# Performance work log

Measured on AMD Instinct MI355X. Metric: run time of the kernel, lower is better.

## Reference

```python
import jax, jax.numpy as jnp
import numpy as np

B, T, E, A = 512, 64, 1536, 6
STOCH, DETER, HID = 32, 512, 512
MIN_STD = 0.1
EPS = 1e-3  # LayerNorm eps in the torch module


def _ln(x, g, b):
    m = jnp.mean(x, -1, keepdims=True)
    v = jnp.var(x, -1, keepdims=True)
    return (x - m) * jax.lax.rsqrt(v + EPS) * g + b


def setup_inputs() -> dict:
    key = jax.random.key(0)
    ks = jax.random.split(key, 20)
    s = 0.02
    f32 = jnp.float32
    return {
        "embed": jax.random.normal(ks[0], (B, T, E), f32),
        "action": jax.random.normal(ks[1], (B, T, A), f32),
        "reset": jnp.zeros((B, T, 1), f32),
        "noise_post": jax.random.normal(ks[2], (T, B, STOCH), f32),
        "noise_prior": jax.random.normal(ks[3], (T, B, STOCH), f32),
        # params
        "W_inp": jax.random.normal(ks[4], (STOCH + A, HID), f32) * s,
        "g_inp": jnp.ones((HID,), f32),
        "b_inp": jnp.zeros((HID,), f32),
        "W_gru": jax.random.normal(ks[5], (HID + DETER, 3 * DETER), f32) * s,
        "W_img": jax.random.normal(ks[6], (DETER, HID), f32) * s,
        "g_img": jnp.ones((HID,), f32),
        "b_img": jnp.zeros((HID,), f32),
        "W_obs": jax.random.normal(ks[7], (DETER + E, HID), f32) * s,
        "g_obs": jnp.ones((HID,), f32),
        "b_obs": jnp.zeros((HID,), f32),
        "W_ims": jax.random.normal(ks[8], (HID, 2 * STOCH), f32) * s,
        "b_ims": jnp.zeros((2 * STOCH,), f32),
        "W_ostat": jax.random.normal(ks[9], (HID, 2 * STOCH), f32) * s,
        "b_ostat": jnp.zeros((2 * STOCH,), f32),
        "W_init": jax.random.normal(ks[10], (1, DETER), f32) * s,
    }


def reference(embed, action, reset, noise_post, noise_prior,
              W_inp, g_inp, b_inp, W_gru, W_img, g_img, b_img,
              W_obs, g_obs, b_obs, W_ims, b_ims, W_ostat, b_ostat, W_init):
    silu = jax.nn.silu

    def img_out(d):
        return silu(_ln(d @ W_img, g_img, b_img))

    def ims_stats(h):
        st = h @ W_ims + b_ims
        mean, std = jnp.split(st, 2, -1)
        return mean, jax.nn.softplus(std) + MIN_STD

    # initial='learned': deter0 = tanh(W); stoch0 = mode of prior dist = mean
    deter0 = jnp.tanh(W_init) * jnp.ones((B, 1), embed.dtype)  # [B, DETER]
    stoch0, _ = ims_stats(img_out(deter0))                     # [B, STOCH]

    def step(carry, xs):
        stoch, deter = carry
        a, e, r, npost, nprior = xs
        # reset handling: blend prev state with initial state
        a = a * (1.0 - r)
        deter = deter * (1.0 - r) + deter0 * r
        stoch = stoch * (1.0 - r) + stoch0 * r
        # img_step: input MLP
        x = silu(_ln(jnp.concatenate([stoch, a], -1) @ W_inp, g_inp, b_inp))
        # GRUCell (update_bias=-1, tanh cand, no norm)
        parts = jnp.concatenate([x, deter], -1) @ W_gru
        rg, cand, up = jnp.split(parts, 3, -1)
        rg = jax.nn.sigmoid(rg)
        cand = jnp.tanh(rg * cand)
        up = jax.nn.sigmoid(up - 1.0)
        deter_n = up * cand + (1.0 - up) * deter
        # prior stats + reparam sample
        p_mean, p_std = ims_stats(img_out(deter_n))
        p_stoch = p_mean + p_std * nprior
        # posterior (temp_post=True: concat deter with embed)
        h = silu(_ln(jnp.concatenate([deter_n, e], -1) @ W_obs, g_obs, b_obs))
        st = h @ W_ostat + b_ostat
        q_mean, q_std = jnp.split(st, 2, -1)
        q_std = jax.nn.softplus(q_std) + MIN_STD
        q_stoch = q_mean + q_std * npost
        out = jnp.concatenate([q_mean, q_std, q_stoch, p_mean, p_std, p_stoch, deter_n], -1)
        return (q_stoch, deter_n), out

    xs = (jnp.swapaxes(action, 0, 1), jnp.swapaxes(embed, 0, 1),
          jnp.swapaxes(reset, 0, 1), noise_post, noise_prior)
    _, outs = jax.lax.scan(step, (stoch0, deter0), xs)
    # [B, T, 6*STOCH + DETER]
    return jnp.swapaxes(outs, 0, 1)
```

## Files before the change

kernel.cpp:

```cpp
#include <hip/hip_runtime.h>
#include <stdint.h>

typedef unsigned short u16;
typedef unsigned int u32;
typedef __attribute__((ext_vector_type(8))) short bf16x8;
typedef __attribute__((ext_vector_type(4))) float f32x4;

#define DEV __device__ __forceinline__

#define NB 512
#define NT 64
#define NE 1536
#define NH 512
#define NS 32

static constexpr size_t OFF_EOBS   = 0;
static constexpr size_t OFF_XX     = OFF_EOBS + (size_t)NT*NB*512*4;
static constexpr size_t OFF_XD     = OFF_XX + (size_t)512*512*2;
static constexpr size_t OFF_DF     = OFF_XD + (size_t)2*512*512*2;
static constexpr size_t OFF_D0     = OFF_DF + (size_t)512*512*4;
static constexpr size_t OFF_S0     = OFF_D0 + 512*4;
static constexpr size_t OFF_WINPT  = OFF_S0 + 256;
static constexpr size_t OFF_WGRUT  = OFF_WINPT + (size_t)512*64*2;
static constexpr size_t OFF_WIMGT  = OFF_WGRUT + (size_t)1536*1024*2;
static constexpr size_t OFF_WOBSDT = OFF_WIMGT + (size_t)512*512*2;
static constexpr size_t OFF_WOBSET = OFF_WOBSDT + (size_t)512*512*2;
static constexpr size_t OFF_WIMST  = OFF_WOBSET + (size_t)512*1536*2;
static constexpr size_t OFF_WOSTT  = OFF_WIMST + (size_t)64*512*2;
static constexpr size_t WS_NEED    = OFF_WOSTT + (size_t)64*512*2;

DEV u16 f2b(float f) {
  u32 u = __builtin_bit_cast(u32, f);
  u32 r = (u + 0x7FFFu + ((u >> 16) & 1u)) >> 16;
  return (u16)r;
}
DEV float b2f(u16 h) { u32 u = (u32)h << 16; return __builtin_bit_cast(float, u); }
DEV u32 pk2(float a, float b) { return (u32)f2b(a) | ((u32)f2b(b) << 16); }
DEV float sigf(float x) { return 1.f / (1.f + __expf(-x)); }
DEV float siluf(float x) { return x * sigf(x); }
DEV float softplusf(float x) { return (x > 20.f) ? x : log1pf(__expf(x)); }
DEV f32x4 mfma16(bf16x8 a, bf16x8 b, f32x4 c) {
  return __builtin_amdgcn_mfma_f32_16x16x32_bf16(a, b, c, 0, 0, 0);
}
DEV size_t bswz(int colgrp, int kkmax, int kk, int lane) {
  return (((size_t)colgrp * kkmax + kk) * 64 + lane) * 8;
}

__global__ __launch_bounds__(256) void k_convert(
    const float* __restrict__ W_inp, const float* __restrict__ W_gru,
    const float* __restrict__ W_img, const float* __restrict__ W_obs,
    const float* __restrict__ W_ims, const float* __restrict__ W_ostat,
    char* __restrict__ ws) {
  u16* winpT  = (u16*)(ws + OFF_WINPT);
  u16* wgruT  = (u16*)(ws + OFF_WGRUT);
  u16* wimgT  = (u16*)(ws + OFF_WIMGT);
  u16* wobsdT = (u16*)(ws + OFF_WOBSDT);
  u16* wobseT = (u16*)(ws + OFF_WOBSET);
  u16* wimsT  = (u16*)(ws + OFF_WIMST);
  u16* wostT  = (u16*)(ws + OFF_WOSTT);
  int o = blockIdx.x * 256 + threadIdx.x;
  if (o < 32768) {
    int i = o & 7, lane = (o >> 3) & 63, rem = o >> 9;
    int kk = rem & 1, cg = rem >> 1;
    int col = cg*16 + (lane & 15), k = kk*32 + (lane >> 4)*8 + i;
    winpT[o] = (k < 38) ? f2b(W_inp[k*512 + col]) : (u16)0;
    return;
  }
  o -= 32768;
  if (o < 1572864) {
    int i = o & 7, lane = (o >> 3) & 63, rem = o >> 9;
    int kk = rem & 31, cg = rem >> 5;
    int col = cg*16 + (lane & 15), k = kk*32 + (lane >> 4)*8 + i;
    wgruT[o] = f2b(W_gru[(size_t)k*1536 + col]);
    return;
  }
  o -= 1572864;
  if (o < 262144) {
    int i = o & 7, lane = (o >> 3) & 63, rem = o >> 9;
    int kk = rem & 15, cg = rem >> 4;
    int col = cg*16 + (lane & 15), k = kk*32 + (lane >> 4)*8 + i;
    wimgT[o] = f2b(W_img[k*512 + col]);
    return;
  }
  o -= 262144;
  if (o < 262144) {
    int i = o & 7, lane = (o >> 3) & 63, rem = o >> 9;
    int kk = rem & 15, cg = rem >> 4;
    int col = cg*16 + (lane & 15), k = kk*32 + (lane >> 4)*8 + i;
    wobsdT[o] = f2b(W_obs[k*512 + col]);
    return;
  }
  o -= 262144;
  if (o < 786432) {
    int i = o & 7, lane = (o >> 3) & 63, rem = o >> 9;
    int kk = rem % 48, cg = rem / 48;
    int col = cg*16 + (lane & 15), k = kk*32 + (lane >> 4)*8 + i;
    wobseT[o] = f2b(W_obs[(size_t)(512 + k)*512 + col]);
    return;
  }
  o -= 786432;
  if (o < 32768) {
    int i = o & 7, lane = (o >> 3) & 63, rem = o >> 9;
    int kk = rem & 15, cg = rem >> 4;
    int col = cg*16 + (lane & 15), k = kk*32 + (lane >> 4)*8 + i;
    wimsT[o] = f2b(W_ims[k*64 + col]);
    return;
  }
  o -= 32768;
  {
    int i = o & 7, lane = (o >> 3) & 63, rem = o >> 9;
    int kk = rem & 15, cg = rem >> 4;
    int col = cg*16 + (lane & 15), k = kk*32 + (lane >> 4)*8 + i;
    wostT[o] = f2b(W_ostat[k*64 + col]);
  }
}

__global__ __launch_bounds__(256) void k_init_a(
    const float* __restrict__ W_init, const float* __restrict__ W_img,
    const float* __restrict__ g_img, const float* __restrict__ b_img,
    const float* __restrict__ W_ims, const float* __restrict__ b_ims,
    char* __restrict__ ws) {
  __shared__ float DL[512];
  __shared__ float HL[512];
  __shared__ float RED[256];
  float* d0 = (float*)(ws + OFF_D0);
  float* s0 = (float*)(ws + OFF_S0);
  const int t = threadIdx.x;
  for (int j = t; j < 512; j += 256) { float v = tanhf(W_init[j]); DL[j] = v; d0[j] = v; }
  __syncthreads();
  float pre0 = 0.f, pre1 = 0.f;
  for (int k = 0; k < 512; ++k) {
    float dv = DL[k];
    pre0 += dv * W_img[k*512 + t];
    pre1 += dv * W_img[k*512 + t + 256];
  }
  RED[t] = pre0 + pre1;
  __syncthreads();
  for (int s = 128; s > 0; s >>= 1) { if (t < s) RED[t] += RED[t + s]; __syncthreads(); }
  float m = RED[0] * (1.f/512.f);
  __syncthreads();
  RED[t] = pre0*pre0 + pre1*pre1;
  __syncthreads();
  for (int s = 128; s > 0; s >>= 1) { if (t < s) RED[t] += RED[t + s]; __syncthreads(); }
  float var = RED[0] * (1.f/512.f) - m*m;
  float inv = rsqrtf(var + 1e-3f);
  HL[t]       = siluf((pre0 - m)*inv*g_img[t] + b_img[t]);
  HL[t + 256] = siluf((pre1 - m)*inv*g_img[t+256] + b_img[t+256]);
  __syncthreads();
  if (t < 32) {
    float s = 0.f;
    for (int k = 0; k < 512; ++k) s += HL[k] * W_ims[k*64 + t];
    s0[t] = s + b_ims[t];
  }
}

__global__ __launch_bounds__(256) void k_phase1(
    const float* __restrict__ embed, char* __restrict__ ws) {
  const u16* wobse = (const u16*)(ws + OFF_WOBSET);
  float* eobs = (float*)(ws + OFF_EOBS);
  __shared__ u16 AL[32 * 40];
  const int tid = threadIdx.x;
  const int mb = blockIdx.x;
  const int w = tid >> 6, l = tid & 63, l15 = l & 15, lk = l >> 4;
  const f32x4 fz = {0.f, 0.f, 0.f, 0.f};
  f32x4 acc[2][8];
  for (int a = 0; a < 2; ++a) for (int f = 0; f < 8; ++f) acc[a][f] = fz;
  const int srow = tid >> 3, sk4 = (tid & 7) * 4;
  const float* abase = embed + (size_t)(mb*32 + srow)*1536 + sk4;
  u16* adst = AL + srow*40 + sk4;
  for (int kk = 0; kk < 48; ++kk) {
    __syncthreads();
    {
      float4 v = *(const float4*)(abase + kk*32);
      uint2 q; q.x = pk2(v.x, v.y); q.y = pk2(v.z, v.w);
      *(uint2*)adst = q;
    }
    __syncthreads();
    bf16x8 af0 = *(const bf16x8*)(AL + l15*40 + lk*8);
    bf16x8 af1 = *(const bf16x8*)(AL + (16 + l15)*40 + lk*8);
    for (int f = 0; f < 8; ++f) {
      bf16x8 bf = *(const bf16x8*)(wobse + bswz(w*8 + f, 48, kk, l));
      acc[0][f] = mfma16(af0, bf, acc[0][f]);
      acc[1][f] = mfma16(af1, bf, acc[1][f]);
    }
  }
  for (int ar = 0; ar < 2; ++ar)
    for (int f = 0; f < 8; ++f) {
      int col = w*128 + f*16 + l15;
      for (int r = 0; r < 4; ++r) {
        int row = mb*32 + ar*16 + lk*4 + r;
        int bb = row >> 6, tt = row & 63;
        __builtin_nontemporal_store(acc[ar][f][r],
            eobs + ((size_t)tt*512 + bb)*512 + col);
      }
    }
}

__global__ __launch_bounds__(512) void k_px0(
    const float* __restrict__ action, const float* __restrict__ reset,
    const float* __restrict__ g_inp, const float* __restrict__ b_inp,
    char* __restrict__ ws) {
  u16* XX = (u16*)(ws + OFF_XX);
  u16* XD0 = (u16*)(ws + OFF_XD);
  float* DF = (float*)(ws + OFF_DF);
  const u16* WINP = (const u16*)(ws + OFF_WINPT);
  const float* d0 = (const float*)(ws + OFF_D0);
  const float* s0 = (const float*)(ws + OFF_S0);
  __shared__ float D0L[512];
  __shared__ float S0L[32];
  __shared__ float STOL[16*32];
  __shared__ float RLC[16];
  __shared__ u16 CIN[16*72];
  __shared__ float LNB[8][16][2];
  const int tid = threadIdx.x;
  const int w = tid >> 6, l = tid & 63, l15 = l & 15, lk = l >> 4;
  const int r0 = blockIdx.x * 16;
  const f32x4 fz = {0.f,0.f,0.f,0.f};
  if (tid < 512) D0L[tid] = d0[tid];
  if (tid < 32) S0L[tid] = s0[tid];
  if (tid < 16) RLC[tid] = reset[(size_t)(r0 + tid)*NT + 0];
  __syncthreads();
  for (int u2 = tid; u2 < 8192; u2 += 512) {
    int rr = u2 >> 9, jj = u2 & 511;
    float v = D0L[jj];
    DF[(size_t)(r0 + rr)*512 + jj] = v;
    XD0[(size_t)(r0 + rr)*512 + jj] = f2b(v);
  }
  if (tid < 512) STOL[tid] = S0L[tid & 31];
  __syncthreads();
  {
    int rr = tid >> 5, kp = (tid & 31)*2;
    float rv = RLC[rr], onem = 1.f - rv;
    int k1 = kp + 1;
    float v0 = (kp < 32) ? (STOL[rr*32+kp]*onem + S0L[kp]*rv)
             : (kp < 38 ? action[((size_t)(r0+rr)*NT + 0)*6 + kp-32]*onem : 0.f);
    float v1 = (k1 < 32) ? (STOL[rr*32+k1]*onem + S0L[k1]*rv)
             : (k1 < 38 ? action[((size_t)(r0+rr)*NT + 0)*6 + k1-32]*onem : 0.f);
    *(u32*)(CIN + rr*72 + kp) = pk2(v0, v1);
  }
  __syncthreads();
  f32x4 ai[4];
  for (int f = 0; f < 4; ++f) ai[f] = fz;
  for (int kk = 0; kk < 2; ++kk) {
    bf16x8 af = *(const bf16x8*)(CIN + l15*72 + kk*32 + lk*8);
    for (int f = 0; f < 4; ++f) {
      bf16x8 bf = *(const bf16x8*)(WINP + bswz(w*4 + f, 2, kk, l));
      ai[f] = mfma16(af, bf, ai[f]);
    }
  }
  for (int r = 0; r < 4; ++r) {
    float s1 = 0.f, s2 = 0.f;
    for (int f = 0; f < 4; ++f) { float v = ai[f][r]; s1 += v; s2 += v*v; }
    for (int d = 1; d < 16; d <<= 1) { s1 += __shfl_xor(s1, d); s2 += __shfl_xor(s2, d); }
    if (l15 == 0) { LNB[w][lk*4 + r][0] = s1; LNB[w][lk*4 + r][1] = s2; }
  }
  __syncthreads();
  float mr[4], ir[4];
  for (int r = 0; r < 4; ++r) {
    int row = lk*4 + r;
    float S1 = 0.f, S2 = 0.f;
    for (int wv = 0; wv < 8; ++wv) { S1 += LNB[wv][row][0]; S2 += LNB[wv][row][1]; }
    float m = S1 * (1.f/512.f);
    float var = S2 * (1.f/512.f) - m*m;
    mr[r] = m; ir[r] = rsqrtf(var + 1e-3f);
  }
  for (int f = 0; f < 4; ++f) {
    int col = w*64 + f*16 + l15;
    float gg = g_inp[col], bb = b_inp[col];
    for (int r = 0; r < 4; ++r)
      XX[(size_t)(r0 + lk*4 + r)*512 + col] = f2b(siluf((ai[f][r] - mr[r]) * ir[r] * gg + bb));
  }
}

__global__ __launch_bounds__(256) void k_gru(
    const float* __restrict__ reset, float* __restrict__ out,
    char* __restrict__ ws, int t) {
  const u16* WGRU = (const u16*)(ws + OFF_WGRUT);
  const u16* XX = (const u16*)(ws + OFF_XX);
  const u16* XDin = (const u16*)(ws + OFF_XD) + (size_t)(t & 1)*512*512;
  u16* XDout = (u16*)(ws + OFF_XD) + (size_t)((t+1) & 1)*512*512;
  float* DF = (float*)(ws + OFF_DF);
  const float* d0 = (const float*)(ws + OFF_D0);
  __shared__ float D0L[512];
  const int tid = threadIdx.x;
  const int w = tid >> 6, l = tid & 63, l15 = l & 15, lk = l >> 4;
  const int g = blockIdx.x >> 5, p = blockIdx.x & 31;
  const int grow0 = g * 64;
  const int jcol = p*16 + l15;
  const f32x4 fz = {0.f,0.f,0.f,0.f};
  for (int u2 = tid; u2 < 512; u2 += 256) D0L[u2] = d0[u2];
  __syncthreads();
  const int arow = grow0 + w*16;
  const float rl = reset[(size_t)(arow + l15)*NT + t];
  const u16* xrow = XX + (size_t)(arow + l15)*512 + lk*8;
  const u16* drow = XDin + (size_t)(arow + l15)*512 + lk*8;
  f32x4 ag0 = fz, ag1 = fz, ag2 = fz;
  #pragma unroll 4
  for (int kk = 0; kk < 16; ++kk) {
    bf16x8 af = *(const bf16x8*)(xrow + kk*32);
    bf16x8 b0 = *(const bf16x8*)(WGRU + bswz(p,      32, kk, l));
    bf16x8 b1 = *(const bf16x8*)(WGRU + bswz(32 + p, 32, kk, l));
    bf16x8 b2 = *(const bf16x8*)(WGRU + bswz(64 + p, 32, kk, l));
    ag0 = mfma16(af, b0, ag0); ag1 = mfma16(af, b1, ag1); ag2 = mfma16(af, b2, ag2);
  }
  #pragma unroll 4
  for (int kk = 0; kk < 16; ++kk) {
    bf16x8 af = *(const bf16x8*)(drow + kk*32);
    if (rl != 0.f) {
      u16* pp = (u16*)&af;
      for (int i = 0; i < 8; ++i)
        pp[i] = f2b(b2f(pp[i])*(1.f - rl) + D0L[kk*32 + lk*8 + i]*rl);
    }
    bf16x8 b0 = *(const bf16x8*)(WGRU + bswz(p,      32, 16 + kk, l));
    bf16x8 b1 = *(const bf16x8*)(WGRU + bswz(32 + p, 32, 16 + kk, l));
    bf16x8 b2 = *(const bf16x8*)(WGRU + bswz(64 + p, 32, 16 + kk, l));
    ag0 = mfma16(af, b0, ag0); ag1 = mfma16(af, b1, ag1); ag2 = mfma16(af, b2, ag2);
  }
  for (int r = 0; r < 4; ++r) {
    int row = arow + lk*4 + r;
    float rr = reset[(size_t)row*NT + t];
    size_t idx = (size_t)row*512 + jcol;
    float dold = DF[idx];
    if (rr != 0.f) dold = dold*(1.f - rr) + D0L[jcol]*rr;
    float rg_ = sigf(ag0[r]);
    float ca = tanhf(rg_ * ag1[r]);
    float up = sigf(ag2[r] - 1.f);
    float dn = up*ca + (1.f - up)*dold;
    DF[idx] = dn;
    XDout[idx] = f2b(dn);
    out[((size_t)row*NT + t)*704 + 192 + jcol] = dn;
  }
}

__global__ __launch_bounds__(512) void k_obs(
    const float* __restrict__ action, const float* __restrict__ reset,
    const float* __restrict__ g_inp, const float* __restrict__ b_inp,
    const float* __restrict__ g_obs, const float* __restrict__ b_obs,
    const float* __restrict__ b_ostat, const float* __restrict__ npost,
    float* __restrict__ out, char* __restrict__ ws, int t) {
  const u16* WOBSD = (const u16*)(ws + OFF_WOBSDT);
  const u16* WOST  = (const u16*)(ws + OFF_WOSTT);
  const u16* WINP  = (const u16*)(ws + OFF_WINPT);
  const float* eobs = (const float*)(ws + OFF_EOBS);
  const u16* XDn = (const u16*)(ws + OFF_XD) + (size_t)((t+1) & 1)*512*512;
  u16* XX = (u16*)(ws + OFF_XX);
  const float* s0 = (const float*)(ws + OFF_S0);
  __shared__ u16 HLDS[16*520];
  __shared__ float LNB[8][16][2];
  __shared__ float STL[16*64];
  __shared__ float STOL[16*32];
  __shared__ float RLC[16];
  __shared__ u16 CIN[16*72];
  __shared__ float S0L[32];
  const int tid = threadIdx.x;
  const int w = tid >> 6, l = tid & 63, l15 = l & 15, lk = l >> 4;
  const int r0 = blockIdx.x * 16;
  const f32x4 fz = {0.f,0.f,0.f,0.f};
  if (tid < 32) S0L[tid] = s0[tid];
  f32x4 ao[4];
  for (int f = 0; f < 4; ++f) ao[f] = fz;
  const u16* abase = XDn + (size_t)(r0 + l15)*512 + lk*8;
  #pragma unroll 4
  for (int kk = 0; kk < 16; ++kk) {
    bf16x8 af = *(const bf16x8*)(abase + kk*32);
    for (int f = 0; f < 4; ++f) {
      bf16x8 bf = *(const bf16x8*)(WOBSD + bswz(w*4 + f, 16, kk, l));
      ao[f] = mfma16(af, bf, ao[f]);
    }
  }
  for (int f = 0; f < 4; ++f) {
    int col = w*64 + f*16 + l15;
    for (int r = 0; r < 4; ++r)
      ao[f][r] += eobs[((size_t)t*512 + r0 + lk*4 + r)*512 + col];
  }
  for (int r = 0; r < 4; ++r) {
    float s1 = 0.f, s2 = 0.f;
    for (int f = 0; f < 4; ++f) { float v = ao[f][r]; s1 += v; s2 += v*v; }
    for (int d = 1; d < 16; d <<= 1) { s1 += __shfl_xor(s1, d); s2 += __shfl_xor(s2, d); }
    if (l15 == 0) { LNB[w][lk*4 + r][0] = s1; LNB[w][lk*4 + r][1] = s2; }
  }
  __syncthreads();
  {
    float mr[4], ir[4];
    for (int r = 0; r < 4; ++r) {
      int row = lk*4 + r;
      float S1 = 0.f, S2 = 0.f;
      for (int wv = 0; wv < 8; ++wv) { S1 += LNB[wv][row][0]; S2 += LNB[wv][row][1]; }
      float m = S1 * (1.f/512.f);
      float var = S2 * (1.f/512.f) - m*m;
      mr[r] = m; ir[r] = rsqrtf(var + 1e-3f);
    }
    for (int f = 0; f < 4; ++f) {
      int col = w*64 + f*16 + l15;
      float gg = g_obs[col], bb = b_obs[col];
      for (int r = 0; r < 4; ++r)
        HLDS[(lk*4 + r)*520 + col] = f2b(siluf((ao[f][r] - mr[r]) * ir[r] * gg + bb));
    }
  }
  __syncthreads();
  if (w < 4) {
    f32x4 q = fz;
    #pragma unroll 4
    for (int kk = 0; kk < 16; ++kk) {
      bf16x8 af = *(const bf16x8*)(HLDS + l15*520 + kk*32 + lk*8);
      bf16x8 bf = *(const bf16x8*)(WOST + bswz(w, 16, kk, l));
      q = mfma16(af, bf, q);
    }
    float bia = b_ostat[w*16 + l15];
    for (int r = 0; r < 4; ++r) STL[(lk*4 + r)*64 + w*16 + l15] = q[r] + bia;
  }
  __syncthreads();
  {
    int row = tid >> 5, i = tid & 31;
    float qm = STL[row*64 + i];
    float qs = softplusf(STL[row*64 + 32 + i]) + 0.1f;
    float ns = npost[((size_t)t*512 + r0 + row)*32 + i];
    float qst = qm + qs*ns;
    size_t ob = ((size_t)(r0 + row)*NT + t)*704;
    out[ob + i] = qm;
    out[ob + 32 + i] = qs;
    out[ob + 64 + i] = qst;
    STOL[row*32 + i] = qst;
  }
  __syncthreads();
  if (t < NT - 1) {
    const int tn = t + 1;
    if (tid < 16) RLC[tid] = reset[(size_t)(r0 + tid)*NT + tn];
    __syncthreads();
    {
      int rr = tid >> 5, kp = (tid & 31)*2;
      float rv = RLC[rr], onem = 1.f - rv;
      int k1 = kp + 1;
      float v0 = (kp < 32) ? (STOL[rr*32+kp]*onem + S0L[kp]*rv)
               : (kp < 38 ? action[((size_t)(r0+rr)*NT + tn)*6 + kp-32]*onem : 0.f);
      float v1 = (k1 < 32) ? (STOL[rr*32+k1]*onem + S0L[k1]*rv)
               : (k1 < 38 ? action[((size_t)(r0+rr)*NT + tn)*6 + k1-32]*onem : 0.f);
      *(u32*)(CIN + rr*72 + kp) = pk2(v0, v1);
    }
    __syncthreads();
    f32x4 ai[4];
    for (int f = 0; f < 4; ++f) ai[f] = fz;
    for (int kk = 0; kk < 2; ++kk) {
      bf16x8 af = *(const bf16x8*)(CIN + l15*72 + kk*32 + lk*8);
      for (int f = 0; f < 4; ++f) {
        bf16x8 bf = *(const bf16x8*)(WINP + bswz(w*4 + f, 2, kk, l));
        ai[f] = mfma16(af, bf, ai[f]);
      }
    }
    for (int r = 0; r < 4; ++r) {
      float s1 = 0.f, s2 = 0.f;
      for (int f = 0; f < 4; ++f) { float v = ai[f][r]; s1 += v; s2 += v*v; }
      for (int d = 1; d < 16; d <<= 1) { s1 += __shfl_xor(s1, d); s2 += __shfl_xor(s2, d); }
      if (l15 == 0) { LNB[w][lk*4 + r][0] = s1; LNB[w][lk*4 + r][1] = s2; }
    }
    __syncthreads();
    float mr[4], ir[4];
    for (int r = 0; r < 4; ++r) {
      int row = lk*4 + r;
      float S1 = 0.f, S2 = 0.f;
      for (int wv = 0; wv < 8; ++wv) { S1 += LNB[wv][row][0]; S2 += LNB[wv][row][1]; }
      float m = S1 * (1.f/512.f);
      float var = S2 * (1.f/512.f) - m*m;
      mr[r] = m; ir[r] = rsqrtf(var + 1e-3f);
    }
    for (int f = 0; f < 4; ++f) {
      int col = w*64 + f*16 + l15;
      float gg = g_inp[col], bb = b_inp[col];
      for (int r = 0; r < 4; ++r)
        XX[(size_t)(r0 + lk*4 + r)*512 + col] = f2b(siluf((ai[f][r] - mr[r]) * ir[r] * gg + bb));
    }
  }
}

__global__ __launch_bounds__(256) void k_p3(
    const float* __restrict__ g_img, const float* __restrict__ b_img,
    const float* __restrict__ b_ims, const float* __restrict__ nprior,
    float* __restrict__ out, char* __restrict__ ws) {
  const u16* wimgT = (const u16*)(ws + OFF_WIMGT);
  const u16* wimsT = (const u16*)(ws + OFF_WIMST);
  __shared__ u16 AL[32 * 40];
  __shared__ u16 HL[32 * 520];
  __shared__ float LNB[4][32][2];
  __shared__ float STL[32 * 64];
  const int tid = threadIdx.x;
  const int mb = blockIdx.x;
  const int w = tid >> 6, l = tid & 63, l15 = l & 15, lk = l >> 4;
  const f32x4 fz = {0.f,0.f,0.f,0.f};
  f32x4 acc[2][8];
  for (int rb = 0; rb < 2; ++rb) for (int f = 0; f < 8; ++f) acc[rb][f] = fz;
  const int srow = tid >> 3, sko = (tid & 7) * 4;
  const float* sbase = out + (size_t)(mb*32 + srow)*704 + 192 + sko;
  u16* sdst = AL + srow*40 + sko;
  for (int kk = 0; kk < 16; ++kk) {
    __syncthreads();
    {
      float4 v = *(const float4*)(sbase + kk*32);
      uint2 q; q.x = pk2(v.x, v.y); q.y = pk2(v.z, v.w);
      *(uint2*)sdst = q;
    }
    __syncthreads();
    bf16x8 af0 = *(const bf16x8*)(AL + l15*40 + lk*8);
    bf16x8 af1 = *(const bf16x8*)(AL + (16 + l15)*40 + lk*8);
    for (int f = 0; f < 8; ++f) {
      bf16x8 bf = *(const bf16x8*)(wimgT + bswz(w*8 + f, 16, kk, l));
      acc[0][f] = mfma16(af0, bf, acc[0][f]);
      acc[1][f] = mfma16(af1, bf, acc[1][f]);
    }
  }
  for (int rb = 0; rb < 2; ++rb) {
    for (int r = 0; r < 4; ++r) {
      float s1 = 0.f, s2 = 0.f;
      for (int f = 0; f < 8; ++f) { float v = acc[rb][f][r]; s1 += v; s2 += v*v; }
      for (int d = 1; d < 16; d <<= 1) { s1 += __shfl_xor(s1, d); s2 += __shfl_xor(s2, d); }
      if (l15 == 0) { LNB[w][rb*16 + lk*4 + r][0] = s1; LNB[w][rb*16 + lk*4 + r][1] = s2; }
    }
  }
  __syncthreads();
  for (int rb = 0; rb < 2; ++rb) {
    float mr[4], ir[4];
    for (int r = 0; r < 4; ++r) {
      int row = rb*16 + lk*4 + r;
      float S1 = LNB[0][row][0] + LNB[1][row][0] + LNB[2][row][0] + LNB[3][row][0];
      float S2 = LNB[0][row][1] + LNB[1][row][1] + LNB[2][row][1] + LNB[3][row][1];
      float m = S1 * (1.f/512.f);
      float var = S2 * (1.f/512.f) - m*m;
      mr[r] = m; ir[r] = rsqrtf(var + 1e-3f);
    }
    for (int f = 0; f < 8; ++f) {
      int col = w*128 + f*16 + l15;
      float gg = g_img[col], bb = b_img[col];
      for (int r = 0; r < 4; ++r) {
        float v = siluf((acc[rb][f][r] - mr[r]) * ir[r] * gg + bb);
        HL[(rb*16 + lk*4 + r)*520 + col] = f2b(v);
      }
    }
  }
  __syncthreads();
  f32x4 q0 = fz, q1 = fz;
  for (int kk = 0; kk < 16; ++kk) {
    bf16x8 bf = *(const bf16x8*)(wimsT + bswz(w, 16, kk, l));
    bf16x8 af0 = *(const bf16x8*)(HL + l15*520 + kk*32 + lk*8);
    bf16x8 af1 = *(const bf16x8*)(HL + (16 + l15)*520 + kk*32 + lk*8);
    q0 = mfma16(af0, bf, q0);
    q1 = mfma16(af1, bf, q1);
  }
  float bia = b_ims[w*16 + l15];
  for (int r = 0; r < 4; ++r) {
    STL[(lk*4 + r)*64 + w*16 + l15] = q0[r] + bia;
    STL[(16 + lk*4 + r)*64 + w*16 + l15] = q1[r] + bia;
  }
  __syncthreads();
  for (int it = tid; it < 1024; it += 256) {
    int row = it >> 5, i = it & 31;
    int grow = mb*32 + row;
    int bb = grow >> 6, tt = grow & 63;
    float pm = STL[row*64 + i];
    float ps = softplusf(STL[row*64 + 32 + i]) + 0.1f;
    float nr = nprior[((size_t)tt*512 + bb)*32 + i];
    float pst = pm + ps*nr;
    size_t ob = (size_t)grow*704;
    out[ob + 96 + i] = pm;
    out[ob + 128 + i] = ps;
    out[ob + 160 + i] = pst;
  }
}

extern "C" void kernel_launch(void* const* d_in, const int* in_sizes, int n_in,
                              void* d_out, int out_size, void* d_ws, size_t ws_size,
                              hipStream_t stream) {
  const float* embed   = (const float*)d_in[0];
  const float* action  = (const float*)d_in[1];
  const float* reset   = (const float*)d_in[2];
  const float* npost   = (const float*)d_in[3];
  const float* nprior  = (const float*)d_in[4];
  const float* W_inp   = (const float*)d_in[5];
  const float* g_inp   = (const float*)d_in[6];
  const float* b_inp   = (const float*)d_in[7];
  const float* W_gru   = (const float*)d_in[8];
  const float* W_img   = (const float*)d_in[9];
  const float* g_img   = (const float*)d_in[10];
  const float* b_img   = (const float*)d_in[11];
  const float* W_obs   = (const float*)d_in[12];
  const float* g_obs   = (const float*)d_in[13];
  const float* b_obs   = (const float*)d_in[14];
  const float* W_ims   = (const float*)d_in[15];
  const float* b_ims   = (const float*)d_in[16];
  const float* W_ostat = (const float*)d_in[17];
  const float* b_ostat = (const float*)d_in[18];
  const float* W_init  = (const float*)d_in[19];
  float* out = (float*)d_out;
  char* ws = (char*)d_ws;
  if (ws_size < WS_NEED) return;

  k_convert<<<11648, 256, 0, stream>>>(W_inp, W_gru, W_img, W_obs, W_ims, W_ostat, ws);
  k_init_a<<<1, 256, 0, stream>>>(W_init, W_img, g_img, b_img, W_ims, b_ims, ws);
  k_phase1<<<1024, 256, 0, stream>>>(embed, ws);
  k_px0<<<32, 512, 0, stream>>>(action, reset, g_inp, b_inp, ws);
  for (int t = 0; t < NT; ++t) {
    k_gru<<<256, 256, 0, stream>>>(reset, out, ws, t);
    k_obs<<<32, 512, 0, stream>>>(action, reset, g_inp, b_inp, g_obs, b_obs,
                                  b_ostat, npost, out, ws, t);
  }
  k_p3<<<1024, 256, 0, stream>>>(g_img, b_img, b_ims, nprior, out, ws);
}
```

Before: 2.546 ms.

## Split per-step obs GEMM into wide kernel, double-buffer A tiles, cache reset

```diff
diff --git a/kernel.cpp b/kernel.cpp
--- a/kernel.cpp
+++ b/kernel.cpp
@@ -18,7 +18,9 @@
 static constexpr size_t OFF_XX     = OFF_EOBS + (size_t)NT*NB*512*4;
 static constexpr size_t OFF_XD     = OFF_XX + (size_t)512*512*2;
 static constexpr size_t OFF_DF     = OFF_XD + (size_t)2*512*512*2;
-static constexpr size_t OFF_D0     = OFF_DF + (size_t)512*512*4;
+static constexpr size_t OFF_ACC    = OFF_DF + (size_t)512*512*4;
+static constexpr size_t OFF_LNP    = OFF_ACC + (size_t)512*512*4;
+static constexpr size_t OFF_D0     = OFF_LNP + (size_t)512*8*2*4;
 static constexpr size_t OFF_S0     = OFF_D0 + 512*4;
 static constexpr size_t OFF_WINPT  = OFF_S0 + 256;
 static constexpr size_t OFF_WGRUT  = OFF_WINPT + (size_t)512*64*2;
@@ -158,7 +160,7 @@
     const float* __restrict__ embed, char* __restrict__ ws) {
   const u16* wobse = (const u16*)(ws + OFF_WOBSET);
   float* eobs = (float*)(ws + OFF_EOBS);
-  __shared__ u16 AL[32 * 40];
+  __shared__ u16 AL[2][32 * 40];
   const int tid = threadIdx.x;
   const int mb = blockIdx.x;
   const int w = tid >> 6, l = tid & 63, l15 = l & 15, lk = l >> 4;
@@ -167,22 +169,29 @@
   for (int a = 0; a < 2; ++a) for (int f = 0; f < 8; ++f) acc[a][f] = fz;
   const int srow = tid >> 3, sk4 = (tid & 7) * 4;
   const float* abase = embed + (size_t)(mb*32 + srow)*1536 + sk4;
-  u16* adst = AL + srow*40 + sk4;
+  const int aoff = srow*40 + sk4;
+  {
+    float4 v = *(const float4*)(abase);
+    uint2 q; q.x = pk2(v.x, v.y); q.y = pk2(v.z, v.w);
+    *(uint2*)(AL[0] + aoff) = q;
+  }
+  float4 vp = *(const float4*)(abase + 32);
+  __syncthreads();
   for (int kk = 0; kk < 48; ++kk) {
-    __syncthreads();
-    {
-      float4 v = *(const float4*)(abase + kk*32);
-      uint2 q; q.x = pk2(v.x, v.y); q.y = pk2(v.z, v.w);
-      *(uint2*)adst = q;
-    }
-    __syncthreads();
-    bf16x8 af0 = *(const bf16x8*)(AL + l15*40 + lk*8);
-    bf16x8 af1 = *(const bf16x8*)(AL + (16 + l15)*40 + lk*8);
+    if (kk < 47) {
+      uint2 q; q.x = pk2(vp.x, vp.y); q.y = pk2(vp.z, vp.w);
+      *(uint2*)(AL[(kk+1)&1] + aoff) = q;
+    }
+    if (kk < 46) vp = *(const float4*)(abase + (kk+2)*32);
+    const u16* ALc = AL[kk&1];
+    bf16x8 af0 = *(const bf16x8*)(ALc + l15*40 + lk*8);
+    bf16x8 af1 = *(const bf16x8*)(ALc + (16 + l15)*40 + lk*8);
     for (int f = 0; f < 8; ++f) {
       bf16x8 bf = *(const bf16x8*)(wobse + bswz(w*8 + f, 48, kk, l));
       acc[0][f] = mfma16(af0, bf, acc[0][f]);
       acc[1][f] = mfma16(af1, bf, acc[1][f]);
     }
+    __syncthreads();
   }
   for (int ar = 0; ar < 2; ++ar)
     for (int f = 0; f < 8; ++f) {
@@ -282,16 +291,18 @@
   float* DF = (float*)(ws + OFF_DF);
   const float* d0 = (const float*)(ws + OFF_D0);
   __shared__ float D0L[512];
+  __shared__ float RL[64];
   const int tid = threadIdx.x;
   const int w = tid >> 6, l = tid & 63, l15 = l & 15, lk = l >> 4;
   const int g = blockIdx.x >> 5, p = blockIdx.x & 31;
   const int grow0 = g * 64;
   const int jcol = p*16 + l15;
   const f32x4 fz = {0.f,0.f,0.f,0.f};
+  if (tid < 64) RL[tid] = reset[(size_t)(grow0 + tid)*NT + t];
   for (int u2 = tid; u2 < 512; u2 += 256) D0L[u2] = d0[u2];
   __syncthreads();
   const int arow = grow0 + w*16;
-  const float rl = reset[(size_t)(arow + l15)*NT + t];
+  const float rl = RL[w*16 + l15];
   const u16* xrow = XX + (size_t)(arow + l15)*512 + lk*8;
   const u16* drow = XDin + (size_t)(arow + l15)*512 + lk*8;
   f32x4 ag0 = fz, ag1 = fz, ag2 = fz;
@@ -318,7 +329,7 @@
   }
   for (int r = 0; r < 4; ++r) {
     int row = arow + lk*4 + r;
-    float rr = reset[(size_t)row*NT + t];
+    float rr = RL[w*16 + lk*4 + r];
     size_t idx = (size_t)row*512 + jcol;
     float dold = DF[idx];
     if (rr != 0.f) dold = dold*(1.f - rr) + D0L[jcol]*rr;
@@ -332,17 +343,58 @@
   }
 }
 
-__global__ __launch_bounds__(512) void k_obs(
+__global__ __launch_bounds__(256) void k_obsA(char* __restrict__ ws, int t) {
+  const u16* WOBSD = (const u16*)(ws + OFF_WOBSDT);
+  const float* eobs = (const float*)(ws + OFF_EOBS);
+  const u16* XDn = (const u16*)(ws + OFF_XD) + (size_t)((t+1) & 1)*512*512;
+  float* ACC = (float*)(ws + OFF_ACC);
+  float* LNP = (float*)(ws + OFF_LNP);
+  __shared__ float LNB[4][16][2];
+  const int tid = threadIdx.x;
+  const int w = tid >> 6, l = tid & 63, l15 = l & 15, lk = l >> 4;
+  const int rg = blockIdx.x >> 3, oc = blockIdx.x & 7;
+  const int cg = oc*4 + w;
+  const f32x4 fz = {0.f,0.f,0.f,0.f};
+  f32x4 ao = fz;
+  const u16* abase = XDn + (size_t)(rg*16 + l15)*512 + lk*8;
+  #pragma unroll 4
+  for (int kk = 0; kk < 16; ++kk) {
+    bf16x8 af = *(const bf16x8*)(abase + kk*32);
+    bf16x8 bf = *(const bf16x8*)(WOBSD + bswz(cg, 16, kk, l));
+    ao = mfma16(af, bf, ao);
+  }
+  const int col = cg*16 + l15;
+  float vs[4];
+  for (int r = 0; r < 4; ++r) {
+    int row = rg*16 + lk*4 + r;
+    float v = ao[r] + eobs[((size_t)t*512 + row)*512 + col];
+    vs[r] = v;
+    ACC[(size_t)row*512 + col] = v;
+  }
+  for (int r = 0; r < 4; ++r) {
+    float s1 = vs[r], s2 = vs[r]*vs[r];
+    for (int d = 1; d < 16; d <<= 1) { s1 += __shfl_xor(s1, d); s2 += __shfl_xor(s2, d); }
+    if (l15 == 0) { LNB[w][lk*4 + r][0] = s1; LNB[w][lk*4 + r][1] = s2; }
+  }
+  __syncthreads();
+  if (tid < 16) {
+    float S1 = LNB[0][tid][0]+LNB[1][tid][0]+LNB[2][tid][0]+LNB[3][tid][0];
+    float S2 = LNB[0][tid][1]+LNB[1][tid][1]+LNB[2][tid][1]+LNB[3][tid][1];
+    LNP[((size_t)(rg*16 + tid)*8 + oc)*2]     = S1;
+    LNP[((size_t)(rg*16 + tid)*8 + oc)*2 + 1] = S2;
+  }
+}
+
+__global__ __launch_bounds__(512) void k_obsB(
     const float* __restrict__ action, const float* __restrict__ reset,
     const float* __restrict__ g_inp, const float* __restrict__ b_inp,
     const float* __restrict__ g_obs, const float* __restrict__ b_obs,
     const float* __restrict__ b_ostat, const float* __restrict__ npost,
     float* __restrict__ out, char* __restrict__ ws, int t) {
-  const u16* WOBSD = (const u16*)(ws + OFF_WOBSDT);
-  const u16* WOST  = (const u16*)(ws + OFF_WOSTT);
-  const u16* WINP  = (const u16*)(ws + OFF_WINPT);
-  const float* eobs = (const float*)(ws + OFF_EOBS);
-  const u16* XDn = (const u16*)(ws + OFF_XD) + (size_t)((t+1) & 1)*512*512;
+  const u16* WOST = (const u16*)(ws + OFF_WOSTT);
+  const u16* WINP = (const u16*)(ws + OFF_WINPT);
+  const float* ACC = (const float*)(ws + OFF_ACC);
+  const float* LNP = (const float*)(ws + OFF_LNP);
   u16* XX = (u16*)(ws + OFF_XX);
   const float* s0 = (const float*)(ws + OFF_S0);
   __shared__ u16 HLDS[16*520];
@@ -352,49 +404,40 @@
   __shared__ float RLC[16];
   __shared__ u16 CIN[16*72];
   __shared__ float S0L[32];
+  __shared__ float MIV[16][2];
   const int tid = threadIdx.x;
   const int w = tid >> 6, l = tid & 63, l15 = l & 15, lk = l >> 4;
   const int r0 = blockIdx.x * 16;
   const f32x4 fz = {0.f,0.f,0.f,0.f};
   if (tid < 32) S0L[tid] = s0[tid];
-  f32x4 ao[4];
-  for (int f = 0; f < 4; ++f) ao[f] = fz;
-  const u16* abase = XDn + (size_t)(r0 + l15)*512 + lk*8;
-  #pragma unroll 4
-  for (int kk = 0; kk < 16; ++kk) {
-    bf16x8 af = *(const bf16x8*)(abase + kk*32);
-    for (int f = 0; f < 4; ++f) {
-      bf16x8 bf = *(const bf16x8*)(WOBSD + bswz(w*4 + f, 16, kk, l));
-      ao[f] = mfma16(af, bf, ao[f]);
-    }
-  }
-  for (int f = 0; f < 4; ++f) {
-    int col = w*64 + f*16 + l15;
-    for (int r = 0; r < 4; ++r)
-      ao[f][r] += eobs[((size_t)t*512 + r0 + lk*4 + r)*512 + col];
-  }
-  for (int r = 0; r < 4; ++r) {
-    float s1 = 0.f, s2 = 0.f;
-    for (int f = 0; f < 4; ++f) { float v = ao[f][r]; s1 += v; s2 += v*v; }
-    for (int d = 1; d < 16; d <<= 1) { s1 += __shfl_xor(s1, d); s2 += __shfl_xor(s2, d); }
-    if (l15 == 0) { LNB[w][lk*4 + r][0] = s1; LNB[w][lk*4 + r][1] = s2; }
+  if (tid < 16) {
+    float S1 = 0.f, S2 = 0.f;
+    for (int o = 0; o < 8; ++o) {
+      S1 += LNP[((size_t)(r0 + tid)*8 + o)*2];
+      S2 += LNP[((size_t)(r0 + tid)*8 + o)*2 + 1];
+    }
+    float m = S1 * (1.f/512.f);
+    float var = S2 * (1.f/512.f) - m*m;
+    MIV[tid][0] = m; MIV[tid][1] = rsqrtf(var + 1e-3f);
   }
   __syncthreads();
   {
-    float mr[4], ir[4];
-    for (int r = 0; r < 4; ++r) {
-      int row = lk*4 + r;
-      float S1 = 0.f, S2 = 0.f;
-      for (int wv = 0; wv < 8; ++wv) { S1 += LNB[wv][row][0]; S2 += LNB[wv][row][1]; }
-      float m = S1 * (1.f/512.f);
-      float var = S2 * (1.f/512.f) - m*m;
-      mr[r] = m; ir[r] = rsqrtf(var + 1e-3f);
-    }
-    for (int f = 0; f < 4; ++f) {
-      int col = w*64 + f*16 + l15;
-      float gg = g_obs[col], bb = b_obs[col];
-      for (int r = 0; r < 4; ++r)
-        HLDS[(lk*4 + r)*520 + col] = f2b(siluf((ao[f][r] - mr[r]) * ir[r] * gg + bb));
+    int row = tid >> 5, c0 = (tid & 31)*16;
+    float m = MIV[row][0], iv = MIV[row][1];
+    const float4* a4 = (const float4*)(ACC + (size_t)(r0+row)*512 + c0);
+    const float4* g4 = (const float4*)(g_obs + c0);
+    const float4* b4 = (const float4*)(b_obs + c0);
+    u16* hrow = HLDS + row*520 + c0;
+    for (int q4 = 0; q4 < 4; ++q4) {
+      float4 av = a4[q4];
+      float4 gv = g4[q4];
+      float4 bv = b4[q4];
+      float v0 = siluf((av.x - m)*iv*gv.x + bv.x);
+      float v1 = siluf((av.y - m)*iv*gv.y + bv.y);
+      float v2 = siluf((av.z - m)*iv*gv.z + bv.z);
+      float v3 = siluf((av.w - m)*iv*gv.w + bv.w);
+      uint2 q; q.x = pk2(v0, v1); q.y = pk2(v2, v3);
+      *(uint2*)(hrow + q4*4) = q;
     }
   }
   __syncthreads();
@@ -478,7 +521,7 @@
     float* __restrict__ out, char* __restrict__ ws) {
   const u16* wimgT = (const u16*)(ws + OFF_WIMGT);
   const u16* wimsT = (const u16*)(ws + OFF_WIMST);
-  __shared__ u16 AL[32 * 40];
+  __shared__ u16 AL[2][32 * 40];
   __shared__ u16 HL[32 * 520];
   __shared__ float LNB[4][32][2];
   __shared__ float STL[32 * 64];
@@ -490,22 +533,29 @@
   for (int rb = 0; rb < 2; ++rb) for (int f = 0; f < 8; ++f) acc[rb][f] = fz;
   const int srow = tid >> 3, sko = (tid & 7) * 4;
   const float* sbase = out + (size_t)(mb*32 + srow)*704 + 192 + sko;
-  u16* sdst = AL + srow*40 + sko;
+  const int aoff = srow*40 + sko;
+  {
+    float4 v = *(const float4*)(sbase);
+    uint2 q; q.x = pk2(v.x, v.y); q.y = pk2(v.z, v.w);
+    *(uint2*)(AL[0] + aoff) = q;
+  }
+  float4 vp = *(const float4*)(sbase + 32);
+  __syncthreads();
   for (int kk = 0; kk < 16; ++kk) {
-    __syncthreads();
-    {
-      float4 v = *(const float4*)(sbase + kk*32);
-      uint2 q; q.x = pk2(v.x, v.y); q.y = pk2(v.z, v.w);
-      *(uint2*)sdst = q;
-    }
-    __syncthreads();
-    bf16x8 af0 = *(const bf16x8*)(AL + l15*40 + lk*8);
-    bf16x8 af1 = *(const bf16x8*)(AL + (16 + l15)*40 + lk*8);
+    if (kk < 15) {
+      uint2 q; q.x = pk2(vp.x, vp.y); q.y = pk2(vp.z, vp.w);
+      *(uint2*)(AL[(kk+1)&1] + aoff) = q;
+    }
+    if (kk < 14) vp = *(const float4*)(sbase + (kk+2)*32);
+    const u16* ALc = AL[kk&1];
+    bf16x8 af0 = *(const bf16x8*)(ALc + l15*40 + lk*8);
+    bf16x8 af1 = *(const bf16x8*)(ALc + (16 + l15)*40 + lk*8);
     for (int f = 0; f < 8; ++f) {
       bf16x8 bf = *(const bf16x8*)(wimgT + bswz(w*8 + f, 16, kk, l));
       acc[0][f] = mfma16(af0, bf, acc[0][f]);
       acc[1][f] = mfma16(af1, bf, acc[1][f]);
     }
+    __syncthreads();
   }
   for (int rb = 0; rb < 2; ++rb) {
     for (int r = 0; r < 4; ++r) {
@@ -598,8 +648,9 @@
   k_px0<<<32, 512, 0, stream>>>(action, reset, g_inp, b_inp, ws);
   for (int t = 0; t < NT; ++t) {
     k_gru<<<256, 256, 0, stream>>>(reset, out, ws, t);
-    k_obs<<<32, 512, 0, stream>>>(action, reset, g_inp, b_inp, g_obs, b_obs,
-                                  b_ostat, npost, out, ws, t);
+    k_obsA<<<256, 256, 0, stream>>>(ws, t);
+    k_obsB<<<32, 512, 0, stream>>>(action, reset, g_inp, b_inp, g_obs, b_obs,
+                                   b_ostat, npost, out, ws, t);
   }
   k_p3<<<1024, 256, 0, stream>>>(g_img, b_img, b_ims, nprior, out, ws);
 }
```

Measured after the change: 2.269 ms. 1.12x faster.
